# Optimization experiments

Hardware: AMD Instinct MI355X
Metric: run time of the kernel (lower is better)

## Reference

```python
import jax, jax.numpy as jnp
import numpy as np

D_MODEL = 256
NHEAD = 4
HEAD_DIM = D_MODEL // NHEAD
TEMP = float(np.sqrt(D_MODEL / NHEAD))
EPS = 1e-5


def layernorm(x, g, b):
    mu = jnp.mean(x, axis=-1, keepdims=True)
    var = jnp.mean(jnp.square(x - mu), axis=-1, keepdims=True)
    return (x - mu) * jax.lax.rsqrt(var + EPS) * g + b


def setup_inputs() -> dict:
    key = jax.random.key(0)
    ks = jax.random.split(key, 8)
    B, S, D = 4, 4096, D_MODEL
    s = 1.0 / np.sqrt(D)
    return {
        "x": jax.random.normal(ks[0], (B, S, D), dtype=jnp.float32),
        "Wq": jax.random.normal(ks[1], (D, D), dtype=jnp.float32) * s,
        "Wk": jax.random.normal(ks[2], (D, D), dtype=jnp.float32) * s,
        "Wv": jax.random.normal(ks[3], (D, D), dtype=jnp.float32) * s,
        "g1": jnp.ones((D,), jnp.float32),
        "b1": jnp.zeros((D,), jnp.float32),
        "g2": jnp.ones((D,), jnp.float32),
        "b2": jnp.zeros((D,), jnp.float32),
        "W1": jax.random.normal(ks[4], (D, D), dtype=jnp.float32) * s,
        "bf1": jnp.zeros((D,), jnp.float32),
        "W2": jax.random.normal(ks[5], (D, D), dtype=jnp.float32) * s,
        "bf2": jnp.zeros((D,), jnp.float32),
    }


def reference(x, Wq, Wk, Wv, g1, b1, g2, b2, W1, bf1, W2, bf2):
    B, S, D = x.shape
    xn = layernorm(x, g1, b1)
    # torch Linear (no bias): y = x @ W.T
    q = (xn @ Wq.T).reshape(B, S, NHEAD, HEAD_DIM)
    k = (xn @ Wk.T).reshape(B, S, NHEAD, HEAD_DIM)
    v = (xn @ Wv.T).reshape(B, S, NHEAD, HEAD_DIM)
    scores = jnp.einsum("bqhd,bkhd->bhqk", q, k) / TEMP
    causal = jnp.tril(jnp.ones((S, S), dtype=bool))  # True = keep
    scores = jnp.where(causal, scores, -jnp.inf)
    attn = jax.nn.softmax(scores, axis=-1)
    att = jnp.einsum("bhqk,bkhd->bqhd", attn, v).reshape(B, S, D)
    xt = x + att
    h = layernorm(xt, g2, b2)
    ffn = jax.nn.relu(h @ W1.T + bf1) @ W2.T + bf2
    return xt + ffn
```

## Files before the change

kernel.cpp:

```cpp
#include <hip/hip_runtime.h>
#include <math.h>

#define D_MODEL 256
#define NHEAD 4
#define HEAD_DIM 64
#define SEQ 4096
#define BATCH 4
#define MROWS (BATCH * SEQ)

typedef __attribute__((ext_vector_type(8))) short short8;
typedef __attribute__((ext_vector_type(4))) short short4v;
typedef __attribute__((ext_vector_type(8))) __bf16 bf16x8;
typedef __attribute__((ext_vector_type(4))) float f32x4;

__device__ inline short f2bf(float f) {
  unsigned u = __float_as_uint(f);
  u += 0x7fffu + ((u >> 16) & 1u);
  return (short)(u >> 16);
}
__device__ inline bf16x8 as_bf8(short8 s) {
  union { short8 s; bf16x8 b; } u;
  u.s = s;
  return u.b;
}
__device__ __forceinline__ void g2lds16(const void* g, void* l) {
  __builtin_amdgcn_global_load_lds(
      (const __attribute__((address_space(1))) unsigned int*)g,
      (__attribute__((address_space(3))) unsigned int*)l, 16, 0, 0);
}

#define QSCALE 0.1803368801111204f

__global__ __launch_bounds__(256) void wcvt(const float* __restrict__ s0, const float* __restrict__ s1,
                                            const float* __restrict__ s2, const float* __restrict__ s3,
                                            const float* __restrict__ s4, short* __restrict__ d0,
                                            short* __restrict__ d1, short* __restrict__ d2,
                                            short* __restrict__ d3, short* __restrict__ d4) {
  int mat = blockIdx.x >> 5;
  int e = ((blockIdx.x & 31) * 256 + threadIdx.x) * 8;
  const float* s = mat == 0 ? s0 : mat == 1 ? s1 : mat == 2 ? s2 : mat == 3 ? s3 : s4;
  short* d = mat == 0 ? d0 : mat == 1 ? d1 : mat == 2 ? d2 : mat == 3 ? d3 : d4;
  int n = e >> 8, k0 = e & 255;
  float4 f0 = *(const float4*)(s + n * 256 + k0);
  float4 f1 = *(const float4*)(s + n * 256 + k0 + 4);
  short8 o = {f2bf(f0.x), f2bf(f0.y), f2bf(f0.z), f2bf(f0.w),
              f2bf(f1.x), f2bf(f1.y), f2bf(f1.z), f2bf(f1.w)};
  int chunk = k0 >> 5, g = (k0 >> 3) & 3;
  *(short8*)(d + n * 256 + chunk * 32 + ((g ^ (n & 3)) * 8)) = o;
}

__global__ __launch_bounds__(256) void ln_sw(const float* __restrict__ x,
                                             const float* __restrict__ g,
                                             const float* __restrict__ b,
                                             short* __restrict__ o) {
  int r = threadIdx.x >> 5, c8 = threadIdx.x & 31;
  int row = blockIdx.x * 8 + r;
  const float* xr = x + (size_t)row * D_MODEL + c8 * 8;
  float4 a = *(const float4*)xr;
  float4 c = *(const float4*)(xr + 4);
  float s = a.x + a.y + a.z + a.w + c.x + c.y + c.z + c.w;
#pragma unroll
  for (int off = 16; off > 0; off >>= 1) s += __shfl_xor(s, off);
  float mu = s * (1.0f / D_MODEL);
  float d0 = a.x - mu, d1 = a.y - mu, d2 = a.z - mu, d3 = a.w - mu;
  float d4 = c.x - mu, d5 = c.y - mu, d6 = c.z - mu, d7 = c.w - mu;
  float ss = d0 * d0 + d1 * d1 + d2 * d2 + d3 * d3 + d4 * d4 + d5 * d5 + d6 * d6 + d7 * d7;
#pragma unroll
  for (int off = 16; off > 0; off >>= 1) ss += __shfl_xor(ss, off);
  float rstd = rsqrtf(ss * (1.0f / D_MODEL) + 1e-5f);
  float4 ga = *(const float4*)(g + c8 * 8);
  float4 gc = *(const float4*)(g + c8 * 8 + 4);
  float4 ba = *(const float4*)(b + c8 * 8);
  float4 bc = *(const float4*)(b + c8 * 8 + 4);
  short8 ov = {f2bf(d0 * rstd * ga.x + ba.x), f2bf(d1 * rstd * ga.y + ba.y),
               f2bf(d2 * rstd * ga.z + ba.z), f2bf(d3 * rstd * ga.w + ba.w),
               f2bf(d4 * rstd * gc.x + bc.x), f2bf(d5 * rstd * gc.y + bc.y),
               f2bf(d6 * rstd * gc.z + bc.z), f2bf(d7 * rstd * gc.w + bc.w)};
  int chunk = c8 >> 2, gr = c8 & 3;
  *(short8*)(o + (size_t)row * D_MODEL + chunk * 32 + ((gr ^ (row & 3)) * 8)) = ov;
}

__global__ __launch_bounds__(256) void qkv_direct(
    const short* __restrict__ Wqi, const short* __restrict__ Wki,
    const short* __restrict__ Wvi, const short* __restrict__ Xn,
    short* __restrict__ qo, short* __restrict__ kimg, short* __restrict__ vimg) {
  __shared__ __align__(16) short Xs[64 * 256];
  const int t = threadIdx.x, lane = t & 63, w = t >> 6;
  const int l15 = lane & 15, quad = lane >> 4;
  const int m0 = blockIdx.x * 64;
  const int which = blockIdx.y;
  const short* Wb = which == 0 ? Wqi : which == 1 ? Wki : Wvi;

#pragma unroll
  for (int j = 0; j < 8; j++) {
    int so = __builtin_amdgcn_readfirstlane((w * 8 + j) * 512);
    g2lds16(Xn + (size_t)m0 * D_MODEL + so + lane * 8, &Xs[so]);
  }
  __syncthreads();

  const short* xb = &Xs[l15 * 256 + ((quad ^ (l15 & 3)) * 8)];
  const short* wb = Wb + (size_t)(w * 64 + l15) * 256 + ((quad ^ (l15 & 3)) * 8);

  f32x4 acc[4][4];
#pragma unroll
  for (int i = 0; i < 4; i++)
#pragma unroll
    for (int j = 0; j < 4; j++) acc[i][j] = (f32x4){0.f, 0.f, 0.f, 0.f};

#pragma unroll
  for (int kf = 0; kf < 8; kf++) {
    bf16x8 fx[4], fw[4];
#pragma unroll
    for (int i = 0; i < 4; i++) {
      fx[i] = as_bf8(*(const short8*)(xb + i * 4096 + kf * 32));
      fw[i] = as_bf8(*(const short8*)(wb + i * 4096 + kf * 32));
    }
    if (which == 2) {
#pragma unroll
      for (int mt = 0; mt < 4; mt++)
#pragma unroll
        for (int nt = 0; nt < 4; nt++)
          acc[mt][nt] = __builtin_amdgcn_mfma_f32_16x16x32_bf16(fx[mt], fw[nt], acc[mt][nt], 0, 0, 0);
    } else {
#pragma unroll
      for (int mt = 0; mt < 4; mt++)
#pragma unroll
        for (int nt = 0; nt < 4; nt++)
          acc[mt][nt] = __builtin_amdgcn_mfma_f32_16x16x32_bf16(fw[nt], fx[mt], acc[mt][nt], 0, 0, 0);
    }
  }

#pragma unroll
  for (int mt = 0; mt < 4; mt++)
#pragma unroll
    for (int nt = 0; nt < 4; nt++) {
      f32x4 v = acc[mt][nt];
      if (which == 2) {
        int n = w * 64 + nt * 16 + l15;
        int mr = m0 + mt * 16 + quad * 4;
        int b = mr >> 12, s = mr & 4095, h = n >> 6, d = n & 63;
        size_t off = ((size_t)(b * NHEAD + h) * 64 + (s >> 6)) * 4096 +
                     (size_t)d * 64 + ((((s & 63) >> 3) ^ (d & 7)) * 8) + (s & 7);
        short4v o = {f2bf(v[0]), f2bf(v[1]), f2bf(v[2]), f2bf(v[3])};
        *(short4v*)(vimg + off) = o;
      } else {
        int m = m0 + mt * 16 + l15;
        int nb = w * 64 + nt * 16 + quad * 4;
        if (which == 0) {
          v *= QSCALE;
          short4v o = {f2bf(v[0]), f2bf(v[1]), f2bf(v[2]), f2bf(v[3])};
          *(short4v*)(qo + (size_t)m * D_MODEL + nb) = o;
        } else {
          int b = m >> 12, s = m & 4095, h = nb >> 6, d = nb & 63;
          size_t off = ((size_t)(b * NHEAD + h) * 64 + (s >> 6)) * 4096 +
                       (size_t)(s & 63) * 64 + (((d >> 3) ^ (s & 7)) * 8) + (d & 7);
          short4v o = {f2bf(v[0]), f2bf(v[1]), f2bf(v[2]), f2bf(v[3])};
          *(short4v*)(kimg + off) = o;
        }
      }
    }
}

__global__ __launch_bounds__(256) void ffn_direct(
    const short* __restrict__ w1i, const short* __restrict__ w2i,
    const short* __restrict__ Hsw, const float* __restrict__ bf1,
    const float* __restrict__ bf2, const float* __restrict__ xt,
    float* __restrict__ out) {
  __shared__ __align__(16) short Hs[32 * 256];
  __shared__ __align__(16) short F1s[32 * 264];
  const int t = threadIdx.x, lane = t & 63, w = t >> 6;
  const int l15 = lane & 15, quad = lane >> 4;
  const int m0 = blockIdx.x * 32;

#pragma unroll
  for (int j = 0; j < 4; j++) {
    int so = __builtin_amdgcn_readfirstlane((w * 4 + j) * 512);
    g2lds16(Hsw + (size_t)m0 * D_MODEL + so + lane * 8, &Hs[so]);
  }
  __syncthreads();

  const short* hb = &Hs[l15 * 256 + ((quad ^ (l15 & 3)) * 8)];
  const short* w1b = w1i + (size_t)(w * 64 + l15) * 256 + ((quad ^ (l15 & 3)) * 8);
  const short* w2b = w2i + (size_t)(w * 64 + l15) * 256 + ((quad ^ (l15 & 3)) * 8);

  f32x4 a1[2][4];
#pragma unroll
  for (int i = 0; i < 2; i++)
#pragma unroll
    for (int j = 0; j < 4; j++) a1[i][j] = (f32x4){0.f, 0.f, 0.f, 0.f};
#pragma unroll
  for (int kf = 0; kf < 8; kf++) {
    bf16x8 fh[2], fw1[4];
#pragma unroll
    for (int i = 0; i < 2; i++) fh[i] = as_bf8(*(const short8*)(hb + i * 4096 + kf * 32));
#pragma unroll
    for (int i = 0; i < 4; i++) fw1[i] = as_bf8(*(const short8*)(w1b + i * 4096 + kf * 32));
#pragma unroll
    for (int mt = 0; mt < 2; mt++)
#pragma unroll
      for (int nt = 0; nt < 4; nt++)
        a1[mt][nt] = __builtin_amdgcn_mfma_f32_16x16x32_bf16(fw1[nt], fh[mt], a1[mt][nt], 0, 0, 0);
  }
#pragma unroll
  for (int mt = 0; mt < 2; mt++)
#pragma unroll
    for (int nt = 0; nt < 4; nt++) {
      int n1 = w * 64 + nt * 16 + quad * 4;
      int ml = mt * 16 + l15;
      float4 bv = *(const float4*)(bf1 + n1);
      f32x4 v = a1[mt][nt];
      short4v o = {f2bf(fmaxf(v[0] + bv.x, 0.f)), f2bf(fmaxf(v[1] + bv.y, 0.f)),
                   f2bf(fmaxf(v[2] + bv.z, 0.f)), f2bf(fmaxf(v[3] + bv.w, 0.f))};
      *(short4v*)&F1s[ml * 264 + n1] = o;
    }
  __syncthreads();

  const short* fb = &F1s[l15 * 264 + quad * 8];
  f32x4 a2[2][4];
#pragma unroll
  for (int i = 0; i < 2; i++)
#pragma unroll
    for (int j = 0; j < 4; j++) a2[i][j] = (f32x4){0.f, 0.f, 0.f, 0.f};
#pragma unroll
  for (int kf = 0; kf < 8; kf++) {
    bf16x8 ff[2], fw2[4];
#pragma unroll
    for (int i = 0; i < 2; i++) ff[i] = as_bf8(*(const short8*)(fb + i * 16 * 264 + kf * 32));
#pragma unroll
    for (int i = 0; i < 4; i++) fw2[i] = as_bf8(*(const short8*)(w2b + i * 4096 + kf * 32));
#pragma unroll
    for (int mt = 0; mt < 2; mt++)
#pragma unroll
      for (int nt = 0; nt < 4; nt++)
        a2[mt][nt] = __builtin_amdgcn_mfma_f32_16x16x32_bf16(ff[mt], fw2[nt], a2[mt][nt], 0, 0, 0);
  }
#pragma unroll
  for (int mt = 0; mt < 2; mt++)
#pragma unroll
    for (int nt = 0; nt < 4; nt++) {
      int n2 = w * 64 + nt * 16 + l15;
      int mg = m0 + mt * 16 + quad * 4;
      float bv = bf2[n2];
      f32x4 v = a2[mt][nt];
#pragma unroll
      for (int r = 0; r < 4; r++) {
        size_t a = (size_t)(mg + r) * D_MODEL + n2;
        out[a] = v[r] + bv + xt[a];
      }
    }
}

__global__ __launch_bounds__(256) void attn_v5(const short* __restrict__ qb,
                                               const short* __restrict__ kimg,
                                               const short* __restrict__ vimg,
                                               const float* __restrict__ x,
                                               float* __restrict__ xt) {
  __shared__ __align__(16) short Ks[2 * 4096];
  __shared__ __align__(16) short Vs[2 * 4096];
  __shared__ __align__(16) short Pt[4][16 * 136];

  const int t = threadIdx.x, lane = t & 63, w = t >> 6;
  const int quad = lane >> 4, l15 = lane & 15, l7 = lane & 7;
  const int qt = 63 - blockIdx.y;
  const int bh = blockIdx.x, b = bh >> 2, h = bh & 3;
  const int ldsoff = __builtin_amdgcn_readfirstlane(w * 512);
  const short* kb_bh = kimg + (size_t)bh * 64 * 4096;
  const short* vb_bh = vimg + (size_t)bh * 64 * 4096;

  const short* kb0 = &Ks[l15 * 64 + ((quad ^ l7) * 8)];
  const short* kb1 = &Ks[l15 * 64 + (((4 + quad) ^ l7) * 8)];
  const short* vb0 = &Vs[l15 * 64 + ((quad ^ l7) * 8)];
  const short* vb1 = &Vs[l15 * 64 + (((4 + quad) ^ l7) * 8)];
  short* pw = &Pt[w][l15 * 136];

  const int q0 = qt * 64;
  const int qrow = q0 + w * 16 + l15;
  const int wq_lo = q0 + w * 16, wq_hi = wq_lo + 15;

  bf16x8 qf0, qf1;
  {
    const short* qp = qb + ((size_t)(b * SEQ + qrow)) * D_MODEL + h * HEAD_DIM + quad * 8;
    qf0 = as_bf8(*(const short8*)qp);
    qf1 = as_bf8(*(const short8*)(qp + 32));
  }
  f32x4 oacc[4];
#pragma unroll
  for (int i = 0; i < 4; i++) oacc[i] = (f32x4){0.f, 0.f, 0.f, 0.f};
  float lrun = 0.f;

  const int niter = (qt + 2) >> 1;

#pragma unroll
  for (int i = 0; i < 4; i++) {
    g2lds16(kb_bh + i * 2048 + t * 8, &Ks[i * 2048 + ldsoff]);
    g2lds16(vb_bh + i * 2048 + t * 8, &Vs[i * 2048 + ldsoff]);
  }
  __syncthreads();

  for (int it = 0; it < niter; it++) {
    const int j0 = it * 128;

    const bool half1 = (j0 + 64) <= wq_hi;
    const int kcmax = half1 ? 8 : 4;
    f32x4 st[8];
#pragma unroll
    for (int kc = 0; kc < 8; kc++) {
      if (kc < kcmax) {
        f32x4 z = (f32x4){0.f, 0.f, 0.f, 0.f};
        bf16x8 kf0 = as_bf8(*(const short8*)(kb0 + (kc & 3) * 1024 + (kc >> 2) * 4096));
        bf16x8 kf1 = as_bf8(*(const short8*)(kb1 + (kc & 3) * 1024 + (kc >> 2) * 4096));
        z = __builtin_amdgcn_mfma_f32_16x16x32_bf16(kf0, qf0, z, 0, 0, 0);
        z = __builtin_amdgcn_mfma_f32_16x16x32_bf16(kf1, qf1, z, 0, 0, 0);
        st[kc] = z;
      }
    }
    if (j0 + 127 > wq_lo) {
#pragma unroll
      for (int kc = 0; kc < 8; kc++)
        if (kc < kcmax) {
#pragma unroll
          for (int r = 0; r < 4; r++)
            if (j0 + kc * 16 + quad * 4 + r > qrow) st[kc][r] = -1e30f;
        }
    }
#pragma unroll
    for (int kc = 0; kc < 8; kc++) {
      if (kc < kcmax) {
#pragma unroll
        for (int r = 0; r < 4; r++) {
          float p = __builtin_amdgcn_exp2f(st[kc][r]);
          st[kc][r] = p;
          lrun += p;
        }
        unsigned u0 = (__float_as_uint(st[kc][0]) >> 16) | (__float_as_uint(st[kc][1]) & 0xffff0000u);
        unsigned u1 = (__float_as_uint(st[kc][2]) >> 16) | (__float_as_uint(st[kc][3]) & 0xffff0000u);
        uint2 uu = {u0, u1};
        *(uint2*)(pw + kc * 16 + quad * 4) = uu;
      }
    }

    __syncthreads();

    if (it + 1 < niter) {
      const short* kc_base = kb_bh + (size_t)(2 * (it + 1)) * 4096;
#pragma unroll
      for (int i = 0; i < 4; i++)
        g2lds16(kc_base + i * 2048 + t * 8, &Ks[i * 2048 + ldsoff]);
    }

    const int fimax = half1 ? 4 : 2;
    bf16x8 pf[4];
#pragma unroll
    for (int fi = 0; fi < 4; fi++)
      if (fi < fimax) pf[fi] = as_bf8(*(const short8*)(pw + fi * 32 + quad * 8));
#pragma unroll
    for (int dt = 0; dt < 4; dt++) {
      f32x4 o = oacc[dt];
#pragma unroll
      for (int fi = 0; fi < 4; fi++) {
        if (fi < fimax) {
          const short* va = (fi & 1) ? vb1 : vb0;
          bf16x8 vf = as_bf8(*(const short8*)(va + dt * 1024 + (fi >> 1) * 4096));
          o = __builtin_amdgcn_mfma_f32_16x16x32_bf16(vf, pf[fi], o, 0, 0, 0);
        }
      }
      oacc[dt] = o;
    }

    __syncthreads();

    if (it + 1 < niter) {
      const short* vc_base = vb_bh + (size_t)(2 * (it + 1)) * 4096;
#pragma unroll
      for (int i = 0; i < 4; i++)
        g2lds16(vc_base + i * 2048 + t * 8, &Vs[i * 2048 + ldsoff]);
    }
  }

  lrun += __shfl_xor(lrun, 16);
  lrun += __shfl_xor(lrun, 32);
  float inv = 1.0f / lrun;
  size_t rowb = ((size_t)(b * SEQ + qrow)) * D_MODEL + h * HEAD_DIM;
#pragma unroll
  for (int dt = 0; dt < 4; dt++) {
    size_t a = rowb + dt * 16 + quad * 4;
    float4 xv = *(const float4*)(x + a);
    float4 o = make_float4(oacc[dt][0] * inv + xv.x, oacc[dt][1] * inv + xv.y,
                           oacc[dt][2] * inv + xv.z, oacc[dt][3] * inv + xv.w);
    *(float4*)(xt + a) = o;
  }
}

extern "C" void kernel_launch(void* const* d_in, const int* in_sizes, int n_in,
                              void* d_out, int out_size, void* d_ws,
                              size_t ws_size, hipStream_t stream) {
  const float* x = (const float*)d_in[0];
  const float* Wq = (const float*)d_in[1];
  const float* Wk = (const float*)d_in[2];
  const float* Wv = (const float*)d_in[3];
  const float* g1 = (const float*)d_in[4];
  const float* b1 = (const float*)d_in[5];
  const float* g2 = (const float*)d_in[6];
  const float* b2 = (const float*)d_in[7];
  const float* W1 = (const float*)d_in[8];
  const float* bf1 = (const float*)d_in[9];
  const float* W2 = (const float*)d_in[10];
  const float* bf2 = (const float*)d_in[11];
  float* out = (float*)d_out;

  char* ws = (char*)d_ws;
  float* xt = (float*)ws;
  short* q_bf = (short*)(ws + (16u << 20));
  short* kimg = (short*)(ws + (24u << 20));
  short* vimg = (short*)(ws + (32u << 20));
  short* xn_sw = (short*)(ws + (40u << 20));
  short* wq_i = (short*)(ws + (48u << 20));
  short* wk_i = wq_i + 65536;
  short* wv_i = wq_i + 2 * 65536;
  short* w1_i = wq_i + 3 * 65536;
  short* w2_i = wq_i + 4 * 65536;

  dim3 blk(256);
  wcvt<<<160, blk, 0, stream>>>(Wq, Wk, Wv, W1, W2, wq_i, wk_i, wv_i, w1_i, w2_i);
  ln_sw<<<MROWS / 8, blk, 0, stream>>>(x, g1, b1, xn_sw);
  qkv_direct<<<dim3(MROWS / 64, 3), blk, 0, stream>>>(wq_i, wk_i, wv_i, xn_sw,
                                                      q_bf, kimg, vimg);
  attn_v5<<<dim3(16, 64), blk, 0, stream>>>(q_bf, kimg, vimg, x, xt);
  ln_sw<<<MROWS / 8, blk, 0, stream>>>(xt, g2, b2, xn_sw);
  ffn_direct<<<MROWS / 32, blk, 0, stream>>>(w1_i, w2_i, xn_sw, bf1, bf2, xt, out);
}
```

Before: 195.8 us.

## Feed softmax probabilities to PV MFMA from registers and interleave causal tile order

The attention kernel no longer stages bf16 probabilities through shared memory. The S^T accumulator layout is reused directly as the B operand of 16x16x16 bf16 MFMAs, with V read in matching 4-element slices. This removes the P store/reload and the per-wave LDS buffer, at the cost of twice as many smaller MFMAs and narrower LDS reads of V. The query-tile order is also permuted across blockIdx.y so that long and short causal tiles are interleaved, which should balance the work across CUs.

```diff
diff --git a/kernel.cpp b/kernel.cpp
--- a/kernel.cpp
+++ b/kernel.cpp
@@ -27,6 +27,15 @@
   __builtin_amdgcn_global_load_lds(
       (const __attribute__((address_space(1))) unsigned int*)g,
       (__attribute__((address_space(3))) unsigned int*)l, 16, 0, 0);
+}
+
+__device__ __forceinline__ f32x4 mfma16bf(short4v a, short4v b, f32x4 c) {
+#if __has_builtin(__builtin_amdgcn_mfma_f32_16x16x16bf16_1k)
+  return __builtin_amdgcn_mfma_f32_16x16x16bf16_1k(a, b, c, 0, 0, 0);
+#else
+  asm("v_mfma_f32_16x16x16_bf16 %0, %1, %2, %0" : "+v"(c) : "v"(a), "v"(b));
+  return c;
+#endif
 }
 
 #define QSCALE 0.1803368801111204f
@@ -250,18 +259,18 @@
     }
 }
 
-__global__ __launch_bounds__(256) void attn_v5(const short* __restrict__ qb,
+__global__ __launch_bounds__(256) void attn_v6(const short* __restrict__ qb,
                                                const short* __restrict__ kimg,
                                                const short* __restrict__ vimg,
                                                const float* __restrict__ x,
                                                float* __restrict__ xt) {
   __shared__ __align__(16) short Ks[2 * 4096];
   __shared__ __align__(16) short Vs[2 * 4096];
-  __shared__ __align__(16) short Pt[4][16 * 136];
 
   const int t = threadIdx.x, lane = t & 63, w = t >> 6;
   const int quad = lane >> 4, l15 = lane & 15, l7 = lane & 7;
-  const int qt = 63 - blockIdx.y;
+  const int yy = blockIdx.y, gq = yy >> 4, rq = yy & 15;
+  const int qt = gq == 0 ? 63 - rq : gq == 1 ? rq : gq == 2 ? 47 - rq : 16 + rq;
   const int bh = blockIdx.x, b = bh >> 2, h = bh & 3;
   const int ldsoff = __builtin_amdgcn_readfirstlane(w * 512);
   const short* kb_bh = kimg + (size_t)bh * 64 * 4096;
@@ -269,9 +278,8 @@
 
   const short* kb0 = &Ks[l15 * 64 + ((quad ^ l7) * 8)];
   const short* kb1 = &Ks[l15 * 64 + (((4 + quad) ^ l7) * 8)];
-  const short* vb0 = &Vs[l15 * 64 + ((quad ^ l7) * 8)];
-  const short* vb1 = &Vs[l15 * 64 + (((4 + quad) ^ l7) * 8)];
-  short* pw = &Pt[w][l15 * 136];
+  const short* vbase = &Vs[l15 * 64 + ((quad & 1) * 4)];
+  const int q1 = quad >> 1;
 
   const int q0 = qt * 64;
   const int qrow = q0 + w * 16 + l15;
@@ -323,19 +331,17 @@
             if (j0 + kc * 16 + quad * 4 + r > qrow) st[kc][r] = -1e30f;
         }
     }
+    uint2 pu[8];
 #pragma unroll
     for (int kc = 0; kc < 8; kc++) {
       if (kc < kcmax) {
-#pragma unroll
-        for (int r = 0; r < 4; r++) {
-          float p = __builtin_amdgcn_exp2f(st[kc][r]);
-          st[kc][r] = p;
-          lrun += p;
-        }
-        unsigned u0 = (__float_as_uint(st[kc][0]) >> 16) | (__float_as_uint(st[kc][1]) & 0xffff0000u);
-        unsigned u1 = (__float_as_uint(st[kc][2]) >> 16) | (__float_as_uint(st[kc][3]) & 0xffff0000u);
-        uint2 uu = {u0, u1};
-        *(uint2*)(pw + kc * 16 + quad * 4) = uu;
+        float p0 = __builtin_amdgcn_exp2f(st[kc][0]);
+        float p1 = __builtin_amdgcn_exp2f(st[kc][1]);
+        float p2 = __builtin_amdgcn_exp2f(st[kc][2]);
+        float p3 = __builtin_amdgcn_exp2f(st[kc][3]);
+        lrun += p0 + p1 + p2 + p3;
+        pu[kc].x = (__float_as_uint(p0) >> 16) | (__float_as_uint(p1) & 0xffff0000u);
+        pu[kc].y = (__float_as_uint(p2) >> 16) | (__float_as_uint(p3) & 0xffff0000u);
       }
     }
 
@@ -348,23 +354,18 @@
         g2lds16(kc_base + i * 2048 + t * 8, &Ks[i * 2048 + ldsoff]);
     }
 
-    const int fimax = half1 ? 4 : 2;
-    bf16x8 pf[4];
-#pragma unroll
-    for (int fi = 0; fi < 4; fi++)
-      if (fi < fimax) pf[fi] = as_bf8(*(const short8*)(pw + fi * 32 + quad * 8));
-#pragma unroll
-    for (int dt = 0; dt < 4; dt++) {
-      f32x4 o = oacc[dt];
-#pragma unroll
-      for (int fi = 0; fi < 4; fi++) {
-        if (fi < fimax) {
-          const short* va = (fi & 1) ? vb1 : vb0;
-          bf16x8 vf = as_bf8(*(const short8*)(va + dt * 1024 + (fi >> 1) * 4096));
-          o = __builtin_amdgcn_mfma_f32_16x16x32_bf16(vf, pf[fi], o, 0, 0, 0);
+#pragma unroll
+    for (int kc = 0; kc < 8; kc++) {
+      if (kc < kcmax) {
+        union { uint2 u; short4v s; } pb;
+        pb.u = pu[kc];
+        const short* vk = vbase + (kc >> 2) * 4096 + (((((kc & 3) * 2) | q1) ^ l7) * 8);
+#pragma unroll
+        for (int dt = 0; dt < 4; dt++) {
+          short4v vv = *(const short4v*)(vk + dt * 1024);
+          oacc[dt] = mfma16bf(vv, pb.s, oacc[dt]);
         }
       }
-      oacc[dt] = o;
     }
 
     __syncthreads();
@@ -425,7 +426,7 @@
   ln_sw<<<MROWS / 8, blk, 0, stream>>>(x, g1, b1, xn_sw);
   qkv_direct<<<dim3(MROWS / 64, 3), blk, 0, stream>>>(wq_i, wk_i, wv_i, xn_sw,
                                                       q_bf, kimg, vimg);
-  attn_v5<<<dim3(16, 64), blk, 0, stream>>>(q_bf, kimg, vimg, x, xt);
+  attn_v6<<<dim3(16, 64), blk, 0, stream>>>(q_bf, kimg, vimg, x, xt);
   ln_sw<<<MROWS / 8, blk, 0, stream>>>(xt, g2, b2, xn_sw);
   ffn_direct<<<MROWS / 32, blk, 0, stream>>>(w1_i, w2_i, xn_sw, bf1, bf2, xt, out);
 }
```

Measured after the change: 199.3 us. No clear change (+1.8%).
